# Performance work log

Measured on AMD Instinct MI355X. Metric: run time of the kernel, lower is better.

The kernel has to match this reference:

```python
import jax, jax.numpy as jnp
import numpy as np

NB_LABELS = 10        # node label alphabet size
NB_EDGE_LABELS = 4    # edge label alphabet size (adjacency values 1..4, 0 = no edge)
N1 = 79               # order of graph 1
N2 = 79               # order of graph 2
NODE_INS_DEL = 0.03
SINKHORN_ITERS = 10


def setup_inputs() -> dict:
    key = jax.random.key(0)
    k1, k2, k3, k4, k5, k6 = jax.random.split(key, 6)
    nb_node_pair = NB_LABELS * (NB_LABELS - 1) // 2      # 45
    nb_edge_pair = NB_EDGE_LABELS * (NB_EDGE_LABELS - 1) // 2  # 6
    node_weights = 0.01 * (1.0 + 0.1 * jax.random.uniform(k1, (nb_node_pair,), dtype=jnp.float32))
    edge_weights = 0.01 * (1.0 + 0.1 * jax.random.uniform(k2, (nb_edge_pair + 1,), dtype=jnp.float32))
    edge_weights = edge_weights.at[-1].set(0.02)
    A_g1 = jax.random.randint(k3, (N1 * N1,), 0, NB_EDGE_LABELS + 1, dtype=jnp.int32)
    A_g2 = jax.random.randint(k4, (N2 * N2,), 0, NB_EDGE_LABELS + 1, dtype=jnp.int32)
    labels_1 = jax.random.randint(k5, (N1,), 0, NB_LABELS, dtype=jnp.int32)
    labels_2 = jax.random.randint(k6, (N2,), 0, NB_LABELS, dtype=jnp.int32)
    return {"A_g1": A_g1, "A_g2": A_g2, "labels_1": labels_1, "labels_2": labels_2,
            "node_weights": node_weights, "edge_weights": edge_weights}


def _symmetric_from_upper(vec, dim):
    iu = jnp.triu_indices(dim, 1)
    M = jnp.zeros((dim, dim), dtype=vec.dtype).at[iu].set(vec)
    return M + M.T


def reference(A_g1, A_g2, labels_1, labels_2, node_weights, edge_weights):
    n, m = labels_1.shape[0], labels_2.shape[0]
    # from_weights_to_costs
    cn = jax.nn.relu(node_weights)
    ce = jax.nn.relu(edge_weights)
    edge_ins_del = ce[-1]
    node_costs = _symmetric_from_upper(cn, NB_LABELS)               # (L_n, L_n)
    edge_costs = _symmetric_from_upper(ce[:-1], NB_EDGE_LABELS)     # (L_e, L_e), zero diagonal
    # Edge-pair cost lookup table over adjacency values 0..L_e.
    # table[a,b] = edge_ins_del if exactly one of a,b is nonzero (ins/del),
    #              edge_costs[a-1,b-1] if both nonzero (substitution; 0 if same label),
    #              0 if both zero. This reproduces edge_ins_del*matrix_edge_ins_del
    # plus the k!=l substitution loop in one gather.
    L = NB_EDGE_LABELS
    table = jnp.zeros((L + 1, L + 1), dtype=cn.dtype)
    table = table.at[1:, 1:].set(edge_costs)
    table = table.at[0, 1:].set(edge_ins_del)
    table = table.at[1:, 0].set(edge_ins_del)
    # Padded adjacency (n+1, n+1) / (m+1, m+1) with a zero dummy row/col.
    A1 = jnp.zeros((n + 1, n + 1), dtype=jnp.int32).at[:n, :n].set(A_g1.reshape(n, n))
    A2 = jnp.zeros((m + 1, m + 1), dtype=jnp.int32).at[:m, :m].set(A_g2.reshape(m, m))
    N = (n + 1) * (m + 1)
    # Kron-style reordering from the unbind/cat trick: C[j*(m+1)+k, i*(m+1)+l] = f(A1[i,j], A2[k,l])
    B1 = A1.T  # B1[j,i] = A1[i,j]
    C = table[B1[:, None, :, None], A2[None, :, None, :]].reshape(N, N)  # (N, N)
    # Diagonal node-cost vector D, index k = i*(m+1)+j
    D2 = jnp.full((n + 1, m + 1), NODE_INS_DEL, dtype=cn.dtype)
    D2 = D2.at[:n, :m].set(node_costs[labels_1[:, None], labels_2[None, :]])
    D2 = D2.at[n, m].set(0.0)
    c = D2.reshape(N)
    idx = jnp.arange(N)
    C = C.at[idx, idx].set(c)        # mask*diag(D) + (1-mask)*C
    Dmat = C.at[idx, idx].set(0.0)   # C - eye*c
    # Sinkhorn on S = exp(-0.5 c), 10 alternating normalizations
    S = jnp.exp(-0.5 * c).reshape(n + 1, m + 1)
    def body(X, _):
        X = X / X.sum(axis=1, keepdims=True)
        X = X / X.sum(axis=0, keepdims=True)
        return X, None
    X, _ = jax.lax.scan(body, S, None, length=SINKHORN_ITERS)
    v = X.reshape(N)
    ged = 0.5 * v @ (Dmat @ v) + c @ v
    return ged
```

## Files before the change

kernel.cpp:

```cpp
#include <hip/hip_runtime.h>
#include <hip/hip_bf16.h>

#define NL 10
#define NE 4
#define N1 79
#define PAD 10
#define NLP 11
#define NODE_INS_DEL 0.03f
#define SINK_ITERS 10

__global__ __launch_bounds__(512) void k_ged(
    const int* __restrict__ Ag1, const int* __restrict__ Ag2,
    const int* __restrict__ l1, const int* __restrict__ l2,
    const float* __restrict__ nw, const float* __restrict__ ew,
    float* __restrict__ dout)
{
    __shared__ float E_ext[121];
    __shared__ float Cc[121];
    __shared__ float T5[25];
    __shared__ float Vm[121];
    __shared__ int   lab1[N1], lab2[N1];
    __shared__ int   cnt1[NLP], cnt2[NLP];
    __shared__ __align__(16) int h1[8][605], h2[8][605];
    __shared__ int   nd1[55], nd2[55];
    __shared__ float M1f[605], M2f[605];
    __shared__ float N1f[55], N2f[55];
    __shared__ float rho[NLP], gam[NLP];
    __shared__ float Ub[605], Yb[605];
    __shared__ float redL[8];

    const int t = threadIdx.x;

    {
        int4* hz1 = (int4*)&h1[0][0];
        int4* hz2 = (int4*)&h2[0][0];
        const int4 z4 = make_int4(0, 0, 0, 0);
        for (int i = t; i < 1210; i += 512) { hz1[i] = z4; hz2[i] = z4; }
    }
    if (t < 55)  nd1[t] = 0;
    if (t >= 55 && t < 110) nd2[t - 55] = 0;
    if (t >= 158 && t < 168) cnt1[t - 158] = 0;
    if (t >= 168 && t < 178) cnt2[t - 168] = 0;
    if (t == 178) cnt1[PAD] = 1;
    if (t == 179) cnt2[PAD] = 1;
    if (t < N1)               lab1[t] = l1[t];
    if (t >= 79 && t < 158)   lab2[t - 79] = l2[t - 79];
    if (t >= 192 && t < 313) {
        int q = t - 192, P = q / 11, S = q - P * 11;
        float cost;
        if (P < NL && S < NL) {
            if (P == S) cost = 0.f;
            else {
                int x = min(P, S), y = max(P, S);
                int pidx = x * (NL - 1) - x * (x - 1) / 2 + (y - x - 1);
                cost = fmaxf(nw[pidx], 0.f);
            }
        } else if (P == PAD && S == PAD) cost = 0.f;
        else cost = NODE_INS_DEL;
        Cc[q] = cost;
        E_ext[q] = __expf(-0.5f * cost);
    }
    if (t >= 320 && t < 345) {
        int q = t - 320, a = q / 5, b = q - a * 5;
        float val;
        if (a == 0 && b == 0)       val = 0.f;
        else if (a == 0 || b == 0)  val = fmaxf(ew[NE * (NE - 1) / 2], 0.f);
        else if (a == b)            val = 0.f;
        else {
            int x = min(a, b) - 1, y = max(a, b) - 1;
            int p = x * (NE - 1) - x * (x - 1) / 2 + (y - x - 1);
            val = fmaxf(ew[p], 0.f);
        }
        T5[q] = val;
    }
    __syncthreads();

    if (t < N1)               atomicAdd(&cnt1[lab1[t]], 1);
    if (t >= 79 && t < 158)   atomicAdd(&cnt2[lab2[t - 79]], 1);
    __syncthreads();

    if (t < 64) {
        const int X = t >> 2, q = t & 3;
        const bool valid = (X < NLP);
        float ec2[3], ec1[3];
        #pragma unroll
        for (int k = 0; k < 3; ++k) {
            int M = 3 * q + k;
            if (valid && M < NLP) {
                float e = E_ext[X * 11 + M];
                ec2[k] = e * (float)cnt2[M];
                ec1[k] = e * (float)cnt1[M];
            } else { ec2[k] = 0.f; ec1[k] = 0.f; }
        }
        const int s0 = 4 * (3 * q + 0);
        const int s1 = 4 * (3 * q + 1);
        const int s2 = (3 * q + 2 < NLP) ? 4 * (3 * q + 2) : 0;
        float gX = 1.0f, rX = 1.0f;
        for (int it = 0; it < SINK_ITERS; ++it) {
            float g0 = __shfl(gX, s0, 64);
            float g1 = __shfl(gX, s1, 64);
            float g2 = __shfl(gX, s2, 64);
            float y = ec2[0] * g0 + ec2[1] * g1 + ec2[2] * g2;
            y += __shfl_xor(y, 1, 64);
            y += __shfl_xor(y, 2, 64);
            rX = valid ? (1.0f / y) : 0.f;
            float r0 = __shfl(rX, s0, 64);
            float r1 = __shfl(rX, s1, 64);
            float r2 = __shfl(rX, s2, 64);
            float z = ec1[0] * r0 + ec1[1] * r1 + ec1[2] * r2;
            z += __shfl_xor(z, 1, 64);
            z += __shfl_xor(z, 2, 64);
            gX = valid ? (1.0f / z) : 0.f;
        }
        if (valid && q == 0) { rho[X] = rX; gam[X] = gX; }
    } else if (t < 288) {
        int* hp = h1[t & 7];
        if (t >= 64 && t < 75)   atomicAdd(&h1[1][(t - 64) * 11 + 10], cnt1[t - 64]);
        if (t >= 80 && t < 90)   atomicAdd(&h1[1][110 + (t - 80)], cnt1[t - 80]);
        if (t >= 96 && t < 107)  atomicAdd(&h2[1][(t - 96) * 11 + 10], cnt2[t - 96]);
        if (t >= 112 && t < 122) atomicAdd(&h2[1][110 + (t - 112)], cnt2[t - 112]);
        if (t >= 64 && t < 64 + N1) {
            int j = t - 64;
            atomicAdd(&nd1[Ag1[j * 80] * 11 + lab1[j]], 1);
        }
        if (t >= 144 && t < 144 + N1) {
            int k = t - 144;
            atomicAdd(&nd2[Ag2[k * 80] * 11 + lab2[k]], 1);
        }
        if (t == 224) nd1[10] = 1;
        if (t == 225) nd2[10] = 1;
        const int q = t - 64;
        #pragma unroll
        for (int itr = 0; itr < 7; ++itr) {
            int m = q + itr * 224;
            if (m < 1560) {
                int4 av = ((const int4*)Ag1)[m];
                int n0 = 4 * m;
                { int n = n0 + 0, i = n / 79, jj = n - i * 79;
                  atomicAdd(&hp[av.x * 121 + lab1[jj] * 11 + lab1[i]], 1); }
                { int n = n0 + 1, i = n / 79, jj = n - i * 79;
                  atomicAdd(&hp[av.y * 121 + lab1[jj] * 11 + lab1[i]], 1); }
                { int n = n0 + 2, i = n / 79, jj = n - i * 79;
                  atomicAdd(&hp[av.z * 121 + lab1[jj] * 11 + lab1[i]], 1); }
                { int n = n0 + 3, i = n / 79, jj = n - i * 79;
                  atomicAdd(&hp[av.w * 121 + lab1[jj] * 11 + lab1[i]], 1); }
            }
        }
        if (t == 64) {
            int a = Ag1[6240];
            atomicAdd(&hp[a * 121 + lab1[78] * 11 + lab1[78]], 1);
        }
    } else {
        int* hp = h2[t & 7];
        const int q = t - 288;
        #pragma unroll
        for (int itr = 0; itr < 7; ++itr) {
            int m = q + itr * 224;
            if (m < 1560) {
                int4 av = ((const int4*)Ag2)[m];
                int n0 = 4 * m;
                { int n = n0 + 0, k = n / 79, ll = n - k * 79;
                  atomicAdd(&hp[av.x * 121 + lab2[k] * 11 + lab2[ll]], 1); }
                { int n = n0 + 1, k = n / 79, ll = n - k * 79;
                  atomicAdd(&hp[av.y * 121 + lab2[k] * 11 + lab2[ll]], 1); }
                { int n = n0 + 2, k = n / 79, ll = n - k * 79;
                  atomicAdd(&hp[av.z * 121 + lab2[k] * 11 + lab2[ll]], 1); }
                { int n = n0 + 3, k = n / 79, ll = n - k * 79;
                  atomicAdd(&hp[av.w * 121 + lab2[k] * 11 + lab2[ll]], 1); }
            }
        }
        if (t == 288) {
            int b = Ag2[6240];
            atomicAdd(&hp[b * 121 + lab2[78] * 11 + lab2[78]], 1);
        }
    }
    __syncthreads();

    for (int i = t; i < 605; i += 512) {
        int s1v = 0, s2v = 0;
        #pragma unroll
        for (int w = 0; w < 8; ++w) { s1v += h1[w][i]; s2v += h2[w][i]; }
        M1f[i] = (float)s1v;
        M2f[i] = (float)s2v;
    }
    if (t < 55) { N1f[t] = (float)nd1[t]; N2f[t] = (float)nd2[t]; }
    if (t >= 64 && t < 185) {
        int q = t - 64;
        Vm[q] = rho[q / 11] * E_ext[q] * gam[q % 11];
    }
    __syncthreads();

    for (int idx = t; idx < 605; idx += 512) {
        int b = idx / 121, r = idx - b * 121;
        int S = r / 11, R = r - S * 11;
        const float* m2 = &M2f[b * 121 + S * 11];
        const float* vr = &Vm[R * 11];
        float s = 0.f;
        #pragma unroll
        for (int T = 0; T < 11; ++T) s = fmaf(m2[T], vr[T], s);
        Ub[idx] = s;
    }
    __syncthreads();

    for (int idx = t; idx < 605; idx += 512) {
        int b = idx / 121, r = idx - b * 121;
        int P = r / 11, R = r - P * 11;
        float s = 0.f;
        #pragma unroll
        for (int S = 0; S < 11; ++S) s = fmaf(Vm[P * 11 + S], Ub[b * 121 + S * 11 + R], s);
        Yb[idx] = s;
    }
    __syncthreads();

    float part = 0.f;
    if (t < 121) {
        int P = t / 11, R = t - P * 11;
        float qf = 0.f;
        #pragma unroll
        for (int a = 0; a < 5; ++a) {
            float sa = 0.f;
            #pragma unroll
            for (int b = 0; b < 5; ++b) sa = fmaf(T5[a * 5 + b], Yb[b * 121 + t], sa);
            qf = fmaf(M1f[a * 121 + t], sa, qf);
        }
        float sd = 0.f;
        #pragma unroll
        for (int a = 0; a < 5; ++a) {
            float sb = 0.f;
            #pragma unroll
            for (int b = 0; b < 5; ++b) sb = fmaf(T5[a * 5 + b], N2f[b * 11 + R], sb);
            sd = fmaf(N1f[a * 11 + P], sb, sd);
        }
        float vv = Vm[t];
        float dpart = vv * vv * sd;
        float cvp = (float)cnt1[P] * (float)cnt2[R] * Cc[t] * vv;
        part = cvp + 0.5f * (qf - dpart);
    }
    #pragma unroll
    for (int off = 1; off < 64; off <<= 1) part += __shfl_xor(part, off, 64);
    if ((t & 63) == 0) redL[t >> 6] = part;
    __syncthreads();
    if (t == 0) {
        float s = 0.f;
        #pragma unroll
        for (int w = 0; w < 8; ++w) s += redL[w];
        dout[0] = s;
    }
}

extern "C" void kernel_launch(void* const* d_in, const int* in_sizes, int n_in,
                              void* d_out, int out_size, void* d_ws, size_t ws_size,
                              hipStream_t stream) {
    const int*   Ag1 = (const int*)d_in[0];
    const int*   Ag2 = (const int*)d_in[1];
    const int*   l1  = (const int*)d_in[2];
    const int*   l2  = (const int*)d_in[3];
    const float* nw  = (const float*)d_in[4];
    const float* ew  = (const float*)d_in[5];
    float* out = (float*)d_out;

    k_ged<<<1, 512, 0, stream>>>(Ag1, Ag2, l1, l2, nw, ew, out);
}
```

Measured before the change: 12.66 us.

## Prefetch adjacency loads early and use padded vectorized LDS layouts

```diff
diff --git a/kernel.cpp b/kernel.cpp
--- a/kernel.cpp
+++ b/kernel.cpp
@@ -19,17 +19,44 @@
     __shared__ float Cc[121];
     __shared__ float T5[25];
     __shared__ float Vm[121];
+    __shared__ __align__(16) float Vm12[132];
     __shared__ int   lab1[N1], lab2[N1];
     __shared__ int   cnt1[NLP], cnt2[NLP];
-    __shared__ __align__(16) int h1[8][605], h2[8][605];
+    __shared__ __align__(16) int h1[605][8], h2[605][8];
     __shared__ int   nd1[55], nd2[55];
-    __shared__ float M1f[605], M2f[605];
+    __shared__ float M1f[605];
+    __shared__ __align__(16) float M2f12[660];
+    __shared__ __align__(16) float UbT12[660];
     __shared__ float N1f[55], N2f[55];
     __shared__ float rho[NLP], gam[NLP];
-    __shared__ float Ub[605], Yb[605];
+    __shared__ float Yb[605];
     __shared__ float redL[8];
 
     const int t = threadIdx.x;
+
+    int4 av[7];
+    int diag1v = 0, diag2v = 0, tailv = 0, lv = 0;
+    if (t >= 64 && t < 288) {
+        const int q = t - 64;
+        #pragma unroll
+        for (int itr = 0; itr < 7; ++itr) {
+            int m = q + itr * 224;
+            av[itr] = (m < 1560) ? ((const int4*)Ag1)[m] : make_int4(0, 0, 0, 0);
+        }
+        if (t < 64 + N1) diag1v = Ag1[(t - 64) * 80];
+        if (t == 64)     tailv  = Ag1[6240];
+    } else if (t >= 288) {
+        const int q = t - 288;
+        #pragma unroll
+        for (int itr = 0; itr < 7; ++itr) {
+            int m = q + itr * 224;
+            av[itr] = (m < 1560) ? ((const int4*)Ag2)[m] : make_int4(0, 0, 0, 0);
+        }
+        if (t == 288) tailv = Ag2[6240];
+    }
+    if (t >= 144 && t < 144 + N1) diag2v = Ag2[(t - 144) * 80];
+    if (t < N1)              { lv = l1[t];      lab1[t] = lv; }
+    if (t >= 79 && t < 158)  { lv = l2[t - 79]; lab2[t - 79] = lv; }
 
     {
         int4* hz1 = (int4*)&h1[0][0];
@@ -43,8 +70,6 @@
     if (t >= 168 && t < 178) cnt2[t - 168] = 0;
     if (t == 178) cnt1[PAD] = 1;
     if (t == 179) cnt2[PAD] = 1;
-    if (t < N1)               lab1[t] = l1[t];
-    if (t >= 79 && t < 158)   lab2[t - 79] = l2[t - 79];
     if (t >= 192 && t < 313) {
         int q = t - 192, P = q / 11, S = q - P * 11;
         float cost;
@@ -75,8 +100,8 @@
     }
     __syncthreads();
 
-    if (t < N1)               atomicAdd(&cnt1[lab1[t]], 1);
-    if (t >= 79 && t < 158)   atomicAdd(&cnt2[lab2[t - 79]], 1);
+    if (t < N1)              atomicAdd(&cnt1[lv], 1);
+    if (t >= 79 && t < 158)  atomicAdd(&cnt2[lv], 1);
     __syncthreads();
 
     if (t < 64) {
@@ -114,19 +139,13 @@
         }
         if (valid && q == 0) { rho[X] = rX; gam[X] = gX; }
     } else if (t < 288) {
-        int* hp = h1[t & 7];
-        if (t >= 64 && t < 75)   atomicAdd(&h1[1][(t - 64) * 11 + 10], cnt1[t - 64]);
-        if (t >= 80 && t < 90)   atomicAdd(&h1[1][110 + (t - 80)], cnt1[t - 80]);
-        if (t >= 96 && t < 107)  atomicAdd(&h2[1][(t - 96) * 11 + 10], cnt2[t - 96]);
-        if (t >= 112 && t < 122) atomicAdd(&h2[1][110 + (t - 112)], cnt2[t - 112]);
-        if (t >= 64 && t < 64 + N1) {
-            int j = t - 64;
-            atomicAdd(&nd1[Ag1[j * 80] * 11 + lab1[j]], 1);
-        }
-        if (t >= 144 && t < 144 + N1) {
-            int k = t - 144;
-            atomicAdd(&nd2[Ag2[k * 80] * 11 + lab2[k]], 1);
-        }
+        const int cp = t & 7;
+        if (t >= 64 && t < 75)   atomicAdd(&h1[(t - 64) * 11 + 10][1], cnt1[t - 64]);
+        if (t >= 80 && t < 90)   atomicAdd(&h1[110 + (t - 80)][1], cnt1[t - 80]);
+        if (t >= 96 && t < 107)  atomicAdd(&h2[(t - 96) * 11 + 10][1], cnt2[t - 96]);
+        if (t >= 112 && t < 122) atomicAdd(&h2[110 + (t - 112)][1], cnt2[t - 112]);
+        if (t >= 64 && t < 64 + N1)  atomicAdd(&nd1[diag1v * 11 + lab1[t - 64]], 1);
+        if (t >= 144 && t < 144 + N1) atomicAdd(&nd2[diag2v * 11 + lab2[t - 144]], 1);
         if (t == 224) nd1[10] = 1;
         if (t == 225) nd2[10] = 1;
         const int q = t - 64;
@@ -134,80 +153,100 @@
         for (int itr = 0; itr < 7; ++itr) {
             int m = q + itr * 224;
             if (m < 1560) {
-                int4 av = ((const int4*)Ag1)[m];
+                int4 a4 = av[itr];
                 int n0 = 4 * m;
                 { int n = n0 + 0, i = n / 79, jj = n - i * 79;
-                  atomicAdd(&hp[av.x * 121 + lab1[jj] * 11 + lab1[i]], 1); }
+                  atomicAdd(&h1[a4.x * 121 + lab1[jj] * 11 + lab1[i]][cp], 1); }
                 { int n = n0 + 1, i = n / 79, jj = n - i * 79;
-                  atomicAdd(&hp[av.y * 121 + lab1[jj] * 11 + lab1[i]], 1); }
+                  atomicAdd(&h1[a4.y * 121 + lab1[jj] * 11 + lab1[i]][cp], 1); }
                 { int n = n0 + 2, i = n / 79, jj = n - i * 79;
-                  atomicAdd(&hp[av.z * 121 + lab1[jj] * 11 + lab1[i]], 1); }
+                  atomicAdd(&h1[a4.z * 121 + lab1[jj] * 11 + lab1[i]][cp], 1); }
                 { int n = n0 + 3, i = n / 79, jj = n - i * 79;
-                  atomicAdd(&hp[av.w * 121 + lab1[jj] * 11 + lab1[i]], 1); }
+                  atomicAdd(&h1[a4.w * 121 + lab1[jj] * 11 + lab1[i]][cp], 1); }
             }
         }
-        if (t == 64) {
-            int a = Ag1[6240];
-            atomicAdd(&hp[a * 121 + lab1[78] * 11 + lab1[78]], 1);
-        }
+        if (t == 64)
+            atomicAdd(&h1[tailv * 121 + lab1[78] * 11 + lab1[78]][cp], 1);
     } else {
-        int* hp = h2[t & 7];
+        const int cp = t & 7;
         const int q = t - 288;
         #pragma unroll
         for (int itr = 0; itr < 7; ++itr) {
             int m = q + itr * 224;
             if (m < 1560) {
-                int4 av = ((const int4*)Ag2)[m];
+                int4 a4 = av[itr];
                 int n0 = 4 * m;
                 { int n = n0 + 0, k = n / 79, ll = n - k * 79;
-                  atomicAdd(&hp[av.x * 121 + lab2[k] * 11 + lab2[ll]], 1); }
+                  atomicAdd(&h2[a4.x * 121 + lab2[k] * 11 + lab2[ll]][cp], 1); }
                 { int n = n0 + 1, k = n / 79, ll = n - k * 79;
-                  atomicAdd(&hp[av.y * 121 + lab2[k] * 11 + lab2[ll]], 1); }
+                  atomicAdd(&h2[a4.y * 121 + lab2[k] * 11 + lab2[ll]][cp], 1); }
                 { int n = n0 + 2, k = n / 79, ll = n - k * 79;
-                  atomicAdd(&hp[av.z * 121 + lab2[k] * 11 + lab2[ll]], 1); }
+                  atomicAdd(&h2[a4.z * 121 + lab2[k] * 11 + lab2[ll]][cp], 1); }
                 { int n = n0 + 3, k = n / 79, ll = n - k * 79;
-                  atomicAdd(&hp[av.w * 121 + lab2[k] * 11 + lab2[ll]], 1); }
+                  atomicAdd(&h2[a4.w * 121 + lab2[k] * 11 + lab2[ll]][cp], 1); }
             }
         }
-        if (t == 288) {
-            int b = Ag2[6240];
-            atomicAdd(&hp[b * 121 + lab2[78] * 11 + lab2[78]], 1);
-        }
+        if (t == 288)
+            atomicAdd(&h2[tailv * 121 + lab2[78] * 11 + lab2[78]][cp], 1);
     }
     __syncthreads();
 
     for (int i = t; i < 605; i += 512) {
-        int s1v = 0, s2v = 0;
-        #pragma unroll
-        for (int w = 0; w < 8; ++w) { s1v += h1[w][i]; s2v += h2[w][i]; }
+        const int4* p1 = (const int4*)&h1[i][0];
+        int4 x0 = p1[0], x1 = p1[1];
+        int s1v = x0.x + x0.y + x0.z + x0.w + x1.x + x1.y + x1.z + x1.w;
         M1f[i] = (float)s1v;
-        M2f[i] = (float)s2v;
-    }
-    if (t < 55) { N1f[t] = (float)nd1[t]; N2f[t] = (float)nd2[t]; }
+        const int4* p2 = (const int4*)&h2[i][0];
+        int4 y0 = p2[0], y1 = p2[1];
+        int s2v = y0.x + y0.y + y0.z + y0.w + y1.x + y1.y + y1.z + y1.w;
+        int b = i / 121, r = i - b * 121, S = r / 11, T = r - S * 11;
+        M2f12[b * 132 + S * 12 + T] = (float)s2v;
+    }
+    if (t < 55) N1f[t] = (float)nd1[t];
+    if (t >= 55 && t < 110) N2f[t - 55] = (float)nd2[t - 55];
     if (t >= 64 && t < 185) {
-        int q = t - 64;
-        Vm[q] = rho[q / 11] * E_ext[q] * gam[q % 11];
-    }
+        int q = t - 64, P = q / 11, R = q - P * 11;
+        float val = rho[P] * E_ext[q] * gam[R];
+        Vm[q] = val;
+        Vm12[P * 12 + R] = val;
+    }
+    if (t >= 256 && t < 311) { int q = t - 256; M2f12[(q / 11) * 132 + (q % 11) * 12 + 11] = 0.f; }
+    if (t >= 311 && t < 366) { int q = t - 311; UbT12[(q / 11) * 132 + (q % 11) * 12 + 11] = 0.f; }
+    if (t >= 366 && t < 377) { Vm12[(t - 366) * 12 + 11] = 0.f; }
     __syncthreads();
 
     for (int idx = t; idx < 605; idx += 512) {
         int b = idx / 121, r = idx - b * 121;
         int S = r / 11, R = r - S * 11;
-        const float* m2 = &M2f[b * 121 + S * 11];
-        const float* vr = &Vm[R * 11];
+        const float4* m2 = (const float4*)&M2f12[b * 132 + S * 12];
+        const float4* vr = (const float4*)&Vm12[R * 12];
+        float4 m0 = m2[0], m1 = m2[1], m2v = m2[2];
+        float4 v0 = vr[0], v1 = vr[1], v2 = vr[2];
         float s = 0.f;
-        #pragma unroll
-        for (int T = 0; T < 11; ++T) s = fmaf(m2[T], vr[T], s);
-        Ub[idx] = s;
+        s = fmaf(m0.x, v0.x, s); s = fmaf(m0.y, v0.y, s);
+        s = fmaf(m0.z, v0.z, s); s = fmaf(m0.w, v0.w, s);
+        s = fmaf(m1.x, v1.x, s); s = fmaf(m1.y, v1.y, s);
+        s = fmaf(m1.z, v1.z, s); s = fmaf(m1.w, v1.w, s);
+        s = fmaf(m2v.x, v2.x, s); s = fmaf(m2v.y, v2.y, s);
+        s = fmaf(m2v.z, v2.z, s); s = fmaf(m2v.w, v2.w, s);
+        UbT12[b * 132 + R * 12 + S] = s;
     }
     __syncthreads();
 
     for (int idx = t; idx < 605; idx += 512) {
         int b = idx / 121, r = idx - b * 121;
         int P = r / 11, R = r - P * 11;
+        const float4* vp = (const float4*)&Vm12[P * 12];
+        const float4* up = (const float4*)&UbT12[b * 132 + R * 12];
+        float4 a0 = vp[0], a1 = vp[1], a2 = vp[2];
+        float4 b0 = up[0], b1 = up[1], b2 = up[2];
         float s = 0.f;
-        #pragma unroll
-        for (int S = 0; S < 11; ++S) s = fmaf(Vm[P * 11 + S], Ub[b * 121 + S * 11 + R], s);
+        s = fmaf(a0.x, b0.x, s); s = fmaf(a0.y, b0.y, s);
+        s = fmaf(a0.z, b0.z, s); s = fmaf(a0.w, b0.w, s);
+        s = fmaf(a1.x, b1.x, s); s = fmaf(a1.y, b1.y, s);
+        s = fmaf(a1.z, b1.z, s); s = fmaf(a1.w, b1.w, s);
+        s = fmaf(a2.x, b2.x, s); s = fmaf(a2.y, b2.y, s);
+        s = fmaf(a2.z, b2.z, s); s = fmaf(a2.w, b2.w, s);
         Yb[idx] = s;
     }
     __syncthreads();
```

Result: slower. 18.40 us (+45.3%).
